# Kernel optimization log

Hardware: AMD Instinct MI355X
Metric: run time of the kernel (lower is better)

## Reference

```python
import jax, jax.numpy as jnp
import numpy as np

BETA = 1.0
EPS = 1e-8  # matches torch F.cosine_similarity eps


def setup_inputs() -> dict:
    key = jax.random.key(0)
    x = jax.random.normal(key, (4096, 2, 1024), dtype=jnp.float32)
    return {"x": x}


def _cosine_sim_matrix(pos, anc):
    # pos: [B, D], anc: [B, D] -> [B, B], sim[i, j] = cos(pos[i], anc[j])
    dots = jnp.einsum('id,jd->ij', pos, anc)
    pn = jnp.sqrt(jnp.sum(pos * pos, axis=-1))
    an = jnp.sqrt(jnp.sum(anc * anc, axis=-1))
    denom = jnp.maximum(pn[:, None] * an[None, :], EPS)
    return dots / denom


def reference(x):
    # x: [B, M, D], M >= 2
    out_anchor = jnp.mean(x[:, 1:, :], axis=1)   # [B, D]
    out_positive = x[:, 0, :]                     # [B, D]
    sim = _cosine_sim_matrix(out_positive, out_anchor)  # [B, B]
    n = sim.shape[0]

    diag = jnp.diagonal(sim)                      # [B]
    # tempsim for column i: beta * (sim[:, i] - sim[i, i]), excluding row i
    T = BETA * (sim - diag[None, :])              # [B, B]
    eye = jnp.eye(n, dtype=bool)

    # exclude-diagonal logsumexp per column (vectorized over all columns)
    Tm = jnp.where(eye, -jnp.inf, T)
    temploss = jax.nn.logsumexp(Tm, axis=0)       # [B]
    # flatNCE trick: exp(l - stop_grad(l)) has value 1 but gradient of l
    nloss = jnp.mean(jnp.exp(temploss - jax.lax.stop_gradient(temploss)))

    # top-1 accuracy against labels arange(B) (detached in original)
    label = jnp.arange(n)
    prec1 = jnp.mean((jnp.argmax(sim, axis=1) == label).astype(jnp.float32)) * 100.0
    return nloss, prec1
```

## Files before the change

kernel.cpp:

```cpp
#include <hip/hip_runtime.h>


#define NROWS 4096
#define DDIM  1024
#define XSTR  2048

typedef unsigned int u32;
typedef unsigned long long u64;
typedef __attribute__((ext_vector_type(8))) short bf16x8;
typedef __attribute__((ext_vector_type(8))) unsigned short u16x8;
typedef __attribute__((ext_vector_type(16))) float f32x16;

__device__ __forceinline__ unsigned int fkey(float f) {
    unsigned int u = __float_as_uint(f);
    return (u & 0x80000000u) ? ~u : (u | 0x80000000u);
}

__device__ __forceinline__ u64 shfl_xor_u64(u64 v, int m) {
    unsigned int lo = (unsigned int)v;
    unsigned int hi = (unsigned int)(v >> 32);
    lo = __shfl_xor(lo, m, 64);
    hi = __shfl_xor(hi, m, 64);
    return ((u64)hi << 32) | lo;
}

__device__ __forceinline__ unsigned short f2bf(float f) {
    unsigned u = __float_as_uint(f);
    return (unsigned short)((u + 0x7FFFu + ((u >> 16) & 1u)) >> 16);
}

#define PF_OFF   0u
#define AF_OFF   8388608u
#define INV_OFF  16777216u
#define PCK_OFF  16793600u
#define DONE_OFF 16826368u
#define WS_NEED  16826432u

__global__ __launch_bounds__(256) void norms2_kernel(const float* __restrict__ x,
                                                     float* __restrict__ inv_an,
                                                     u64* __restrict__ packed,
                                                     unsigned int* __restrict__ done) {
    int gid  = blockIdx.x * 256 + threadIdx.x;
    int j    = gid >> 6;
    int lane = threadIdx.x & 63;
    if (gid < NROWS) packed[gid] = 0ULL;
    if (gid == 0) *done = 0u;
    const float4* a = (const float4*)(x + (size_t)j * XSTR + DDIM);
    float s = 0.0f;
#pragma unroll
    for (int i = 0; i < 4; ++i) {
        float4 v = a[lane + i * 64];
        s += v.x * v.x + v.y * v.y + v.z * v.z + v.w * v.w;
    }
#pragma unroll
    for (int off = 32; off > 0; off >>= 1) s += __shfl_down(s, off, 64);
    if (lane == 0) inv_an[j] = 1.0f / sqrtf(s);
}

__global__ __launch_bounds__(256) void conv_kernel(const float* __restrict__ x,
                                                   unsigned short* __restrict__ Pf,
                                                   unsigned short* __restrict__ Af) {
    const int cid  = blockIdx.x * 256 + threadIdx.x;
    const int lane = cid & 63;
    const int kh   = (cid >> 6) & 63;
    const int fb   = cid >> 12;
    const int row  = fb * 32 + (lane & 31);
    const int col  = kh * 16 + (lane >> 5) * 8;

    const float* px = x + (size_t)row * XSTR + col;
    float4 p0 = *(const float4*)(px);
    float4 p1 = *(const float4*)(px + 4);
    float4 a0 = *(const float4*)(px + DDIM);
    float4 a1 = *(const float4*)(px + DDIM + 4);

    u16x8 pv, av;
    pv[0] = f2bf(p0.x); pv[1] = f2bf(p0.y); pv[2] = f2bf(p0.z); pv[3] = f2bf(p0.w);
    pv[4] = f2bf(p1.x); pv[5] = f2bf(p1.y); pv[6] = f2bf(p1.z); pv[7] = f2bf(p1.w);
    av[0] = f2bf(a0.x); av[1] = f2bf(a0.y); av[2] = f2bf(a0.z); av[3] = f2bf(a0.w);
    av[4] = f2bf(a1.x); av[5] = f2bf(a1.y); av[6] = f2bf(a1.z); av[7] = f2bf(a1.w);

    *(u16x8*)(Pf + (size_t)cid * 8) = pv;
    *(u16x8*)(Af + (size_t)cid * 8) = av;
}

__global__ __launch_bounds__(512, 2) void mfma_gemm_argmax(const unsigned short* __restrict__ Pf,
                                                           const unsigned short* __restrict__ Af,
                                                           const float* __restrict__ inv_an,
                                                           u64* __restrict__ packed,
                                                           unsigned int* __restrict__ done,
                                                           float* __restrict__ out) {
    __shared__ __align__(16) unsigned int lds[32768];
    __shared__ unsigned int lastflag;
    __shared__ int cnt[8];

    const int bid = blockIdx.x;
    const int xcd = bid & 7;
    const int slt = bid >> 3;
    const int rblk = (xcd >> 1) * 4 + (slt >> 3);
    const int cblk = (xcd & 1) * 8 + (slt & 7);
    const int r0 = rblk * 256;
    const int c0 = cblk * 256;

    const int wave = threadIdx.x >> 6;
    const int lane = threadIdx.x & 63;
    const int l31 = lane & 31;
    const int lh = lane >> 5;
    const int wm = wave & 3;
    const int wn = wave >> 2;

    const char* gPs = (const char*)Pf + (((size_t)(rblk * 8 + wave)) << 16) + (size_t)lane * 16;
    const char* gAs = (const char*)Af + (((size_t)(cblk * 8 + wave)) << 16) + (size_t)lane * 16;

    f32x16 zero16 = {0.f,0.f,0.f,0.f,0.f,0.f,0.f,0.f,0.f,0.f,0.f,0.f,0.f,0.f,0.f,0.f};
    f32x16 acc[2][4];
#pragma unroll
    for (int i = 0; i < 2; ++i)
#pragma unroll
        for (int j = 0; j < 4; ++j) acc[i][j] = zero16;

#pragma unroll
    for (int kh_l = 0; kh_l < 4; ++kh_l) {
        __builtin_amdgcn_global_load_lds((const u32*)(gPs + ((size_t)kh_l << 10)),
                                         &lds[kh_l * 2048 + wave * 256], 16, 0, 0);
        __builtin_amdgcn_global_load_lds((const u32*)(gAs + ((size_t)kh_l << 10)),
                                         &lds[8192 + kh_l * 2048 + wave * 256], 16, 0, 0);
    }

    for (int t = 0; t < 16; ++t) {
        const int cb = t & 1;
        const int cbuf = cb * 16384;
        const int nbuf = (cb ^ 1) * 16384;

        asm volatile("s_waitcnt vmcnt(0)" ::: "memory");
        __builtin_amdgcn_s_barrier();
        __builtin_amdgcn_sched_barrier(0);

        if (t + 1 < 16) {
#pragma unroll
            for (int kh_l = 0; kh_l < 4; ++kh_l) {
                const size_t go = ((size_t)((t + 1) * 4 + kh_l)) << 10;
                __builtin_amdgcn_global_load_lds((const u32*)(gPs + go),
                                                 &lds[nbuf + kh_l * 2048 + wave * 256], 16, 0, 0);
                __builtin_amdgcn_global_load_lds((const u32*)(gAs + go),
                                                 &lds[nbuf + 8192 + kh_l * 2048 + wave * 256], 16, 0, 0);
            }
        }

        __builtin_amdgcn_s_setprio(1);
#pragma unroll
        for (int kh_l = 0; kh_l < 4; ++kh_l) {
            const u32* bp = &lds[cbuf + kh_l * 2048 + (wm * 2) * 256 + lane * 4];
            bf16x8 f_p0 = *(const bf16x8*)(bp);
            bf16x8 f_p1 = *(const bf16x8*)(bp + 256);
            const u32* ba = &lds[cbuf + 8192 + kh_l * 2048 + (wn * 4) * 256 + lane * 4];
            bf16x8 f_a0 = *(const bf16x8*)(ba);
            bf16x8 f_a1 = *(const bf16x8*)(ba + 256);
            bf16x8 f_a2 = *(const bf16x8*)(ba + 512);
            bf16x8 f_a3 = *(const bf16x8*)(ba + 768);

            acc[0][0] = __builtin_amdgcn_mfma_f32_32x32x16_bf16(f_p0, f_a0, acc[0][0], 0, 0, 0);
            acc[0][1] = __builtin_amdgcn_mfma_f32_32x32x16_bf16(f_p0, f_a1, acc[0][1], 0, 0, 0);
            acc[0][2] = __builtin_amdgcn_mfma_f32_32x32x16_bf16(f_p0, f_a2, acc[0][2], 0, 0, 0);
            acc[0][3] = __builtin_amdgcn_mfma_f32_32x32x16_bf16(f_p0, f_a3, acc[0][3], 0, 0, 0);
            acc[1][0] = __builtin_amdgcn_mfma_f32_32x32x16_bf16(f_p1, f_a0, acc[1][0], 0, 0, 0);
            acc[1][1] = __builtin_amdgcn_mfma_f32_32x32x16_bf16(f_p1, f_a1, acc[1][1], 0, 0, 0);
            acc[1][2] = __builtin_amdgcn_mfma_f32_32x32x16_bf16(f_p1, f_a2, acc[1][2], 0, 0, 0);
            acc[1][3] = __builtin_amdgcn_mfma_f32_32x32x16_bf16(f_p1, f_a3, acc[1][3], 0, 0, 0);
        }
        __builtin_amdgcn_s_setprio(0);
    }

    float ian[4];
#pragma unroll
    for (int nt = 0; nt < 4; ++nt) ian[nt] = inv_an[c0 + wn * 128 + nt * 32 + l31];

#pragma unroll
    for (int mt = 0; mt < 2; ++mt)
#pragma unroll
        for (int reg = 0; reg < 16; ++reg) {
            const int row = r0 + wm * 64 + mt * 32 + (reg & 3) + 8 * (reg >> 2) + 4 * lh;
            u64 best = 0ULL;
#pragma unroll
            for (int nt = 0; nt < 4; ++nt) {
                const int col = c0 + wn * 128 + nt * 32 + l31;
                const float v = acc[mt][nt][reg] * ian[nt];
                const u64 p = ((u64)fkey(v) << 32) | (unsigned int)(~col);
                best = best > p ? best : p;
            }
#pragma unroll
            for (int m = 1; m <= 16; m <<= 1) {
                const u64 o = shfl_xor_u64(best, m);
                best = best > o ? best : o;
            }
            if (l31 == 0) atomicMax(&packed[row], best);
        }

    __syncthreads();
    if (threadIdx.x == 0) {
        __threadfence();
        unsigned int old = atomicAdd(done, 1u);
        lastflag = (old == 255u) ? 1u : 0u;
    }
    __syncthreads();
    if (lastflag) {
        int c = 0;
        for (int r = threadIdx.x; r < NROWS; r += 512) {
            u64 v = atomicAdd(&packed[r], 0ULL);
            unsigned int col = ~(unsigned int)(v & 0xFFFFFFFFULL);
            c += (col == (unsigned int)r) ? 1 : 0;
        }
#pragma unroll
        for (int off = 32; off > 0; off >>= 1) c += __shfl_down(c, off, 64);
        if ((threadIdx.x & 63) == 0) cnt[threadIdx.x >> 6] = c;
        __syncthreads();
        if (threadIdx.x == 0) {
            int tot = 0;
#pragma unroll
            for (int w = 0; w < 8; ++w) tot += cnt[w];
            out[0] = 1.0f;
            out[1] = 100.0f * (float)tot / (float)NROWS;
        }
    }
}

__global__ __launch_bounds__(256) void norms_kernel(const float* __restrict__ x,
                                                    float* __restrict__ inv_an,
                                                    u64* __restrict__ packed) {
    int gid  = blockIdx.x * 256 + threadIdx.x;
    int j    = gid >> 6;
    int lane = threadIdx.x & 63;
    if (gid < NROWS) packed[gid] = 0ULL;
    const float4* a = (const float4*)(x + (size_t)j * XSTR + DDIM);
    float s = 0.0f;
#pragma unroll
    for (int i = 0; i < 4; ++i) {
        float4 v = a[lane + i * 64];
        s += v.x * v.x + v.y * v.y + v.z * v.z + v.w * v.w;
    }
#pragma unroll
    for (int off = 32; off > 0; off >>= 1) s += __shfl_down(s, off, 64);
    if (lane == 0) inv_an[j] = 1.0f / sqrtf(s);
}

__global__ __launch_bounds__(256) void gemm_argmax_kernel(const float* __restrict__ x,
                                                          const float* __restrict__ inv_an,
                                                          u64* __restrict__ packed) {
    __shared__ __align__(16) float Pt[16][128];
    __shared__ __align__(16) float At[16][128];
    const int r0 = blockIdx.x * 128;
    const int c0 = blockIdx.y * 128;
    const int t = threadIdx.x;
    const int tx = t & 15;
    const int ty = t >> 4;
    const int srow = t >> 1;
    const int skq = (t & 1) * 8;
    float acc[8][8];
#pragma unroll
    for (int r = 0; r < 8; ++r)
#pragma unroll
        for (int c = 0; c < 8; ++c) acc[r][c] = 0.0f;
    const float* gp = x + (size_t)(r0 + srow) * XSTR + skq;
    const float* ga = x + (size_t)(c0 + srow) * XSTR + DDIM + skq;
    for (int k0 = 0; k0 < DDIM; k0 += 16) {
        __syncthreads();
        float4 p0 = *(const float4*)(gp + k0);
        float4 p1 = *(const float4*)(gp + k0 + 4);
        float4 a0 = *(const float4*)(ga + k0);
        float4 a1 = *(const float4*)(ga + k0 + 4);
        Pt[skq + 0][srow] = p0.x; Pt[skq + 1][srow] = p0.y;
        Pt[skq + 2][srow] = p0.z; Pt[skq + 3][srow] = p0.w;
        Pt[skq + 4][srow] = p1.x; Pt[skq + 5][srow] = p1.y;
        Pt[skq + 6][srow] = p1.z; Pt[skq + 7][srow] = p1.w;
        At[skq + 0][srow] = a0.x; At[skq + 1][srow] = a0.y;
        At[skq + 2][srow] = a0.z; At[skq + 3][srow] = a0.w;
        At[skq + 4][srow] = a1.x; At[skq + 5][srow] = a1.y;
        At[skq + 6][srow] = a1.z; At[skq + 7][srow] = a1.w;
        __syncthreads();
#pragma unroll
        for (int kk = 0; kk < 16; ++kk) {
            float pr[8], ar[8];
            *(float4*)&pr[0] = *(const float4*)&Pt[kk][ty * 8];
            *(float4*)&pr[4] = *(const float4*)&Pt[kk][ty * 8 + 4];
            *(float4*)&ar[0] = *(const float4*)&At[kk][tx * 8];
            *(float4*)&ar[4] = *(const float4*)&At[kk][tx * 8 + 4];
#pragma unroll
            for (int r = 0; r < 8; ++r)
#pragma unroll
                for (int c = 0; c < 8; ++c) acc[r][c] += pr[r] * ar[c];
        }
    }
    float ian[8];
#pragma unroll
    for (int c = 0; c < 8; ++c) ian[c] = inv_an[c0 + tx * 8 + c];
#pragma unroll
    for (int r = 0; r < 8; ++r) {
        int row = r0 + ty * 8 + r;
        u64 best = 0ULL;
#pragma unroll
        for (int c = 0; c < 8; ++c) {
            int col = c0 + tx * 8 + c;
            float v = acc[r][c] * ian[c];
            u64 p = ((u64)fkey(v) << 32) | (unsigned int)(~col);
            best = best > p ? best : p;
        }
#pragma unroll
        for (int m = 1; m <= 8; m <<= 1) {
            u64 o = shfl_xor_u64(best, m);
            best = best > o ? best : o;
        }
        if (tx == 0) atomicMax(&packed[row], best);
    }
}

__global__ __launch_bounds__(256) void finalize_kernel(const u64* __restrict__ packed,
                                                       float* __restrict__ out) {
    __shared__ int cnt_s;
    int t = threadIdx.x;
    if (t == 0) cnt_s = 0;
    __syncthreads();
    int c = 0;
    for (int r = t; r < NROWS; r += 256) {
        unsigned int col = ~(unsigned int)(packed[r] & 0xFFFFFFFFULL);
        c += (col == (unsigned int)r) ? 1 : 0;
    }
#pragma unroll
    for (int off = 32; off > 0; off >>= 1) c += __shfl_down(c, off, 64);
    if ((t & 63) == 0) atomicAdd(&cnt_s, c);
    __syncthreads();
    if (t == 0) {
        out[0] = 1.0f;
        out[1] = 100.0f * (float)cnt_s / (float)NROWS;
    }
}

extern "C" void kernel_launch(void* const* d_in, const int* in_sizes, int n_in,
                              void* d_out, int out_size, void* d_ws, size_t ws_size,
                              hipStream_t stream) {
    (void)in_sizes; (void)n_in; (void)out_size;
    const float* x = (const float*)d_in[0];
    float* out = (float*)d_out;

    if (ws_size >= (size_t)WS_NEED) {
        char* ws = (char*)d_ws;
        unsigned short* Pf = (unsigned short*)(ws + PF_OFF);
        unsigned short* Af = (unsigned short*)(ws + AF_OFF);
        float* inv_an = (float*)(ws + INV_OFF);
        u64* packed = (u64*)(ws + PCK_OFF);
        unsigned int* done = (unsigned int*)(ws + DONE_OFF);

        norms2_kernel<<<NROWS / 4, 256, 0, stream>>>(x, inv_an, packed, done);
        conv_kernel<<<2048, 256, 0, stream>>>(x, Pf, Af);
        mfma_gemm_argmax<<<256, 512, 0, stream>>>(Pf, Af, inv_an, packed, done, out);
    } else {
        float* inv_an = (float*)d_ws;
        u64* packed = (u64*)((char*)d_ws + NROWS * sizeof(float));
        norms_kernel<<<NROWS / 4, 256, 0, stream>>>(x, inv_an, packed);
        dim3 grid(NROWS / 128, NROWS / 128);
        gemm_argmax_kernel<<<grid, 256, 0, stream>>>(x, inv_an, packed);
        finalize_kernel<<<1, 256, 0, stream>>>(packed, out);
    }
}
```

Baseline: 123.3 us.

## Deepen GEMM prefetch to four-stage ring with smaller K tiles and ping-pong phases

Replaces the double-buffered 64-deep K tile loop with a 4-slot ring of 32-deep K tiles, keeping three tiles in flight and waiting with partial vmcnt counts instead of draining all loads each step. Each half-tile compute phase is bracketed by barriers with priority raised around the MFMA burst, a ping-pong style schedule between waves. The intent is to hide global-to-LDS latency behind MFMA work. In exchange it adds more barriers per K step and relies on the vmcnt arithmetic matching exactly four loads per tile.

```diff
diff --git a/kernel.cpp b/kernel.cpp
--- a/kernel.cpp
+++ b/kernel.cpp
@@ -118,56 +118,63 @@
 #pragma unroll
         for (int j = 0; j < 4; ++j) acc[i][j] = zero16;
 
-#pragma unroll
-    for (int kh_l = 0; kh_l < 4; ++kh_l) {
-        __builtin_amdgcn_global_load_lds((const u32*)(gPs + ((size_t)kh_l << 10)),
-                                         &lds[kh_l * 2048 + wave * 256], 16, 0, 0);
-        __builtin_amdgcn_global_load_lds((const u32*)(gAs + ((size_t)kh_l << 10)),
-                                         &lds[8192 + kh_l * 2048 + wave * 256], 16, 0, 0);
-    }
-
-    for (int t = 0; t < 16; ++t) {
-        const int cb = t & 1;
-        const int cbuf = cb * 16384;
-        const int nbuf = (cb ^ 1) * 16384;
-
-        asm volatile("s_waitcnt vmcnt(0)" ::: "memory");
+#define ISSUE_TILE(tt)                                                                  \
+    {                                                                                   \
+        const int sb_ = ((tt) & 3) * 8192;                                              \
+        const size_t go_ = ((size_t)((tt) * 2)) << 10;                                  \
+        __builtin_amdgcn_global_load_lds((const u32*)(gPs + go_),                       \
+                                         &lds[sb_ + wave * 256], 16, 0, 0);             \
+        __builtin_amdgcn_global_load_lds((const u32*)(gAs + go_),                       \
+                                         &lds[sb_ + 4096 + wave * 256], 16, 0, 0);      \
+        __builtin_amdgcn_global_load_lds((const u32*)(gPs + go_ + 1024),                \
+                                         &lds[sb_ + 2048 + wave * 256], 16, 0, 0);      \
+        __builtin_amdgcn_global_load_lds((const u32*)(gAs + go_ + 1024),                \
+                                         &lds[sb_ + 4096 + 2048 + wave * 256], 16, 0, 0);\
+    }
+
+#define PHASE(kh_l)                                                                     \
+    {                                                                                   \
+        const u32* bp_ = &lds[cbuf + (kh_l) * 2048 + (wm * 2) * 256 + lane * 4];        \
+        bf16x8 f_p0 = *(const bf16x8*)(bp_);                                            \
+        bf16x8 f_p1 = *(const bf16x8*)(bp_ + 256);                                      \
+        const u32* ba_ = &lds[cbuf + 4096 + (kh_l) * 2048 + (wn * 4) * 256 + lane * 4]; \
+        bf16x8 f_a0 = *(const bf16x8*)(ba_);                                            \
+        bf16x8 f_a1 = *(const bf16x8*)(ba_ + 256);                                      \
+        bf16x8 f_a2 = *(const bf16x8*)(ba_ + 512);                                      \
+        bf16x8 f_a3 = *(const bf16x8*)(ba_ + 768);                                      \
+        __builtin_amdgcn_s_barrier();                                                   \
+        asm volatile("s_waitcnt lgkmcnt(0)" ::: "memory");                              \
+        __builtin_amdgcn_sched_barrier(0);                                              \
+        __builtin_amdgcn_s_setprio(1);                                                  \
+        acc[0][0] = __builtin_amdgcn_mfma_f32_32x32x16_bf16(f_p0, f_a0, acc[0][0], 0, 0, 0); \
+        acc[0][1] = __builtin_amdgcn_mfma_f32_32x32x16_bf16(f_p0, f_a1, acc[0][1], 0, 0, 0); \
+        acc[0][2] = __builtin_amdgcn_mfma_f32_32x32x16_bf16(f_p0, f_a2, acc[0][2], 0, 0, 0); \
+        acc[0][3] = __builtin_amdgcn_mfma_f32_32x32x16_bf16(f_p0, f_a3, acc[0][3], 0, 0, 0); \
+        acc[1][0] = __builtin_amdgcn_mfma_f32_32x32x16_bf16(f_p1, f_a0, acc[1][0], 0, 0, 0); \
+        acc[1][1] = __builtin_amdgcn_mfma_f32_32x32x16_bf16(f_p1, f_a1, acc[1][1], 0, 0, 0); \
+        acc[1][2] = __builtin_amdgcn_mfma_f32_32x32x16_bf16(f_p1, f_a2, acc[1][2], 0, 0, 0); \
+        acc[1][3] = __builtin_amdgcn_mfma_f32_32x32x16_bf16(f_p1, f_a3, acc[1][3], 0, 0, 0); \
+        __builtin_amdgcn_s_setprio(0);                                                  \
+        __builtin_amdgcn_s_barrier();                                                   \
+    }
+
+    ISSUE_TILE(0)
+    ISSUE_TILE(1)
+    ISSUE_TILE(2)
+
+    for (int t = 0; t < 32; ++t) {
+        const int cbuf = (t & 3) * 8192;
+
+        if (t + 3 < 32) ISSUE_TILE(t + 3)
+
+        if      (t < 29)  asm volatile("s_waitcnt vmcnt(12)" ::: "memory");
+        else if (t == 29) asm volatile("s_waitcnt vmcnt(8)" ::: "memory");
+        else if (t == 30) asm volatile("s_waitcnt vmcnt(4)" ::: "memory");
+        else              asm volatile("s_waitcnt vmcnt(0)" ::: "memory");
         __builtin_amdgcn_s_barrier();
-        __builtin_amdgcn_sched_barrier(0);
-
-        if (t + 1 < 16) {
-#pragma unroll
-            for (int kh_l = 0; kh_l < 4; ++kh_l) {
-                const size_t go = ((size_t)((t + 1) * 4 + kh_l)) << 10;
-                __builtin_amdgcn_global_load_lds((const u32*)(gPs + go),
-                                                 &lds[nbuf + kh_l * 2048 + wave * 256], 16, 0, 0);
-                __builtin_amdgcn_global_load_lds((const u32*)(gAs + go),
-                                                 &lds[nbuf + 8192 + kh_l * 2048 + wave * 256], 16, 0, 0);
-            }
-        }
-
-        __builtin_amdgcn_s_setprio(1);
-#pragma unroll
-        for (int kh_l = 0; kh_l < 4; ++kh_l) {
-            const u32* bp = &lds[cbuf + kh_l * 2048 + (wm * 2) * 256 + lane * 4];
-            bf16x8 f_p0 = *(const bf16x8*)(bp);
-            bf16x8 f_p1 = *(const bf16x8*)(bp + 256);
-            const u32* ba = &lds[cbuf + 8192 + kh_l * 2048 + (wn * 4) * 256 + lane * 4];
-            bf16x8 f_a0 = *(const bf16x8*)(ba);
-            bf16x8 f_a1 = *(const bf16x8*)(ba + 256);
-            bf16x8 f_a2 = *(const bf16x8*)(ba + 512);
-            bf16x8 f_a3 = *(const bf16x8*)(ba + 768);
-
-            acc[0][0] = __builtin_amdgcn_mfma_f32_32x32x16_bf16(f_p0, f_a0, acc[0][0], 0, 0, 0);
-            acc[0][1] = __builtin_amdgcn_mfma_f32_32x32x16_bf16(f_p0, f_a1, acc[0][1], 0, 0, 0);
-            acc[0][2] = __builtin_amdgcn_mfma_f32_32x32x16_bf16(f_p0, f_a2, acc[0][2], 0, 0, 0);
-            acc[0][3] = __builtin_amdgcn_mfma_f32_32x32x16_bf16(f_p0, f_a3, acc[0][3], 0, 0, 0);
-            acc[1][0] = __builtin_amdgcn_mfma_f32_32x32x16_bf16(f_p1, f_a0, acc[1][0], 0, 0, 0);
-            acc[1][1] = __builtin_amdgcn_mfma_f32_32x32x16_bf16(f_p1, f_a1, acc[1][1], 0, 0, 0);
-            acc[1][2] = __builtin_amdgcn_mfma_f32_32x32x16_bf16(f_p1, f_a2, acc[1][2], 0, 0, 0);
-            acc[1][3] = __builtin_amdgcn_mfma_f32_32x32x16_bf16(f_p1, f_a3, acc[1][3], 0, 0, 0);
-        }
-        __builtin_amdgcn_s_setprio(0);
+
+        PHASE(0)
+        PHASE(1)
     }
 
     float ian[4];
@@ -221,6 +228,8 @@
             out[1] = 100.0f * (float)tot / (float)NROWS;
         }
     }
+#undef ISSUE_TILE
+#undef PHASE
 }
 
 __global__ __launch_bounds__(256) void norms_kernel(const float* __restrict__ x,
```

Result: slower. 131.2 us (+6.4%).
